# Kernel optimization log

Measured on AMD Instinct MI355X. Metric: run time of the kernel, lower is better.

Reference implementation:

```python
import jax, jax.numpy as jnp
import numpy as np

B_SZ, L, N, H = 8, 4096, 256, 256
R_MIN, R_MAX, MAX_PHASE = 0.0, 1.0, 0.314


def setup_inputs() -> dict:
    key = jax.random.key(0)
    ks = jax.random.split(key, 8)
    x = jax.random.normal(ks[0], (B_SZ, L, H), jnp.float32)
    def glorot(k, shape):
        return jax.random.normal(k, shape, jnp.float32) * jnp.sqrt(2.0 / (shape[0] + shape[1])).astype(jnp.float32)
    B_re = glorot(ks[1], (N, H))
    B_im = glorot(ks[2], (N, H))
    C_re = glorot(ks[3], (H, N))
    C_im = glorot(ks[4], (H, N))
    # DiskRingRadius / DiskRingPhase initializers
    u1 = jax.random.uniform(ks[5], (N,), jnp.float32, 1e-6, 1.0)
    u2 = jax.random.uniform(ks[6], (N,), jnp.float32, 1e-6, 1.0)
    nu_log = jnp.log(-0.5 * jnp.log(u1 * (R_MAX ** 2 - R_MIN ** 2) + R_MIN ** 2))
    theta_log = jnp.log(MAX_PHASE * u2)
    D = jax.random.normal(ks[7], (H,), jnp.float32) * 0.05  # RandomNormal(stddev=0.05)
    return dict(x=x, B_re=B_re, B_im=B_im, C_re=C_re, C_im=C_im,
                nu_log=nu_log, theta_log=theta_log, D=D)


def reference(x, B_re, B_im, C_re, C_im, nu_log, theta_log, D):
    # Diagonal complex recurrence parameters
    Lambda = jnp.exp(jax.lax.complex(-jnp.exp(nu_log), jnp.exp(theta_log)))  # [N]
    gamma = jnp.sqrt(1.0 - jnp.abs(Lambda) ** 2).astype(jnp.complex64)       # [N]
    B_norm = (B_re + 1j * B_im).astype(jnp.complex64) * gamma[:, None]       # [N,H]
    C = (C_re + 1j * C_im).astype(jnp.complex64)                             # [H,N]

    # Input projection: [B,L,N] complex
    Bu = jnp.einsum('blh,nh->bln', x.astype(jnp.complex64), B_norm)
    Lambda_el = jnp.broadcast_to(Lambda, Bu.shape)

    def combine(a, b):
        la, ba = a
        lb, bb = b
        return (la * lb, lb * ba + bb)

    _, states = jax.lax.associative_scan(combine, (Lambda_el, Bu), axis=1)  # [B,L,N]

    y = jnp.real(jnp.einsum('bln,hn->blh', states, C))
    y = y + x * D  # H_in == H -> elementwise skip
    return y
```

## Files before the change

### kernel.cpp

```cpp
#include <hip/hip_runtime.h>
#include <hip/hip_bf16.h>
#include <math.h>

#define B_SZ 8
#define LSEQ 4096
#define NDIM 256
#define HDIM 256
#define MROWS (B_SZ * LSEQ)
#define CH 64
#define NC (LSEQ / CH)

#define BM 64
#define BN 128
#define BK 32
#define PAD 40
#define SSTR 68

typedef _Float16 half8 __attribute__((ext_vector_type(8)));
typedef _Float16 half4 __attribute__((ext_vector_type(4)));
typedef float fx4 __attribute__((ext_vector_type(4)));

__global__ void k_prep(const float* __restrict__ Bre, const float* __restrict__ Bim,
                       const float* __restrict__ Cre, const float* __restrict__ Cim,
                       const float* __restrict__ nu_log, const float* __restrict__ th_log,
                       _Float16* __restrict__ BreH, _Float16* __restrict__ BimH,
                       _Float16* __restrict__ CreH, _Float16* __restrict__ CimNH,
                       float* __restrict__ lamRe, float* __restrict__ lamIm,
                       float* __restrict__ powRe, float* __restrict__ powIm) {
    int r = blockIdx.x;
    int t = threadIdx.x;
    float nu  = expf(nu_log[r]);
    float th  = expf(th_log[r]);
    float mod = expf(-nu);
    float g   = sqrtf(fmaxf(1.0f - mod * mod, 0.0f));
    if (t == 0) {
        lamRe[r] = mod * cosf(th);
        lamIm[r] = mod * sinf(th);
    }
    int i = r * 256 + t;
    BreH[i]  = (_Float16)(Bre[i] * g);
    BimH[i]  = (_Float16)(Bim[i] * g);
    CreH[i]  = (_Float16)Cre[i];
    CimNH[i] = (_Float16)(-Cim[i]);
    if (r < CH) {
        float nuN = expf(nu_log[t]);
        float thN = expf(th_log[t]);
        float k   = (float)(r + 1);
        float mo  = expf(-nuN * k);
        powRe[r * 256 + t] = mo * cosf(thN * k);
        powIm[r * 256 + t] = mo * sinf(thN * k);
    }
}

__launch_bounds__(256)
__global__ void k_buscan(const float* __restrict__ x,
                         const _Float16* __restrict__ BreH,
                         const _Float16* __restrict__ BimH,
                         const float* __restrict__ lamRe,
                         const float* __restrict__ lamIm,
                         _Float16* __restrict__ stReH,
                         _Float16* __restrict__ stImH,
                         float* __restrict__ finRe,
                         float* __restrict__ finIm) {
    __shared__ __align__(16) _Float16 smem[25600];

    const int tid  = threadIdx.x;
    const int lane = tid & 63;
    const int wave = tid >> 6;
    const int wr   = wave >> 1;
    const int wc   = wave & 1;
    const int m0   = blockIdx.x * BM;
    const int n0   = blockIdx.y * BN;

    const int ar = tid >> 2, ac = (tid & 3) * 8;
    const int br = tid >> 1, bc = (tid & 1) * 16;

    const int fRC = lane & 15;
    const int fKg = (lane >> 4) * 8;

    fx4 accR[8], accI[8];
#pragma unroll
    for (int i = 0; i < 8; ++i) { accR[i] = (fx4)0.0f; accI[i] = (fx4)0.0f; }

    float4 xf0, xf1;
    half8 w0, w1, w2, w3;

    {
        const float* xp = x + (size_t)(m0 + ar) * HDIM + ac;
        xf0 = *(const float4*)xp;
        xf1 = *(const float4*)(xp + 4);
        const _Float16* bp1 = BreH + (size_t)(n0 + br) * HDIM + bc;
        const _Float16* bp2 = BimH + (size_t)(n0 + br) * HDIM + bc;
        w0 = *(const half8*)bp1;  w1 = *(const half8*)(bp1 + 8);
        w2 = *(const half8*)bp2;  w3 = *(const half8*)(bp2 + 8);
        half8 hv;
        hv[0]=(_Float16)xf0.x; hv[1]=(_Float16)xf0.y; hv[2]=(_Float16)xf0.z; hv[3]=(_Float16)xf0.w;
        hv[4]=(_Float16)xf1.x; hv[5]=(_Float16)xf1.y; hv[6]=(_Float16)xf1.z; hv[7]=(_Float16)xf1.w;
        *(half8*)&smem[ar * PAD + ac] = hv;
        *(half8*)&smem[2560 + br * PAD + bc] = w0;  *(half8*)&smem[2560 + br * PAD + bc + 8] = w1;
        *(half8*)&smem[7680 + br * PAD + bc] = w2;  *(half8*)&smem[7680 + br * PAD + bc + 8] = w3;
    }
    __syncthreads();

    int p = 0;
    for (int k0 = 0; k0 < HDIM; k0 += BK) {
        const int po = p * 12800;
        const bool nx = (k0 + BK) < HDIM;
        if (nx) {
            const float* xp = x + (size_t)(m0 + ar) * HDIM + k0 + BK + ac;
            xf0 = *(const float4*)xp;
            xf1 = *(const float4*)(xp + 4);
            const _Float16* bp1 = BreH + (size_t)(n0 + br) * HDIM + k0 + BK + bc;
            const _Float16* bp2 = BimH + (size_t)(n0 + br) * HDIM + k0 + BK + bc;
            w0 = *(const half8*)bp1;  w1 = *(const half8*)(bp1 + 8);
            w2 = *(const half8*)bp2;  w3 = *(const half8*)(bp2 + 8);
        }
        half8 af[2], bRf[4], bIf[4];
#pragma unroll
        for (int sm = 0; sm < 2; ++sm)
            af[sm] = *(const half8*)&smem[po + (wr * 32 + sm * 16 + fRC) * PAD + fKg];
#pragma unroll
        for (int sn = 0; sn < 4; ++sn) {
            bRf[sn] = *(const half8*)&smem[po + 2560 + (wc * 64 + sn * 16 + fRC) * PAD + fKg];
            bIf[sn] = *(const half8*)&smem[po + 7680 + (wc * 64 + sn * 16 + fRC) * PAD + fKg];
        }
#pragma unroll
        for (int sm = 0; sm < 2; ++sm)
#pragma unroll
            for (int sn = 0; sn < 4; ++sn) {
                accR[sm * 4 + sn] = __builtin_amdgcn_mfma_f32_16x16x32_f16(af[sm], bRf[sn], accR[sm * 4 + sn], 0, 0, 0);
                accI[sm * 4 + sn] = __builtin_amdgcn_mfma_f32_16x16x32_f16(af[sm], bIf[sn], accI[sm * 4 + sn], 0, 0, 0);
            }
        if (nx) {
            const int qo = (p ^ 1) * 12800;
            half8 hv;
            hv[0]=(_Float16)xf0.x; hv[1]=(_Float16)xf0.y; hv[2]=(_Float16)xf0.z; hv[3]=(_Float16)xf0.w;
            hv[4]=(_Float16)xf1.x; hv[5]=(_Float16)xf1.y; hv[6]=(_Float16)xf1.z; hv[7]=(_Float16)xf1.w;
            *(half8*)&smem[qo + ar * PAD + ac] = hv;
            *(half8*)&smem[qo + 2560 + br * PAD + bc] = w0;  *(half8*)&smem[qo + 2560 + br * PAD + bc + 8] = w1;
            *(half8*)&smem[qo + 7680 + br * PAD + bc] = w2;  *(half8*)&smem[qo + 7680 + br * PAD + bc + 8] = w3;
        }
        __syncthreads();
        p ^= 1;
    }

    _Float16* SRe = smem;
    _Float16* SIm = smem + 8704;

    const int rBase = (lane >> 4) * 4;
#pragma unroll
    for (int sm = 0; sm < 2; ++sm)
#pragma unroll
        for (int sn = 0; sn < 4; ++sn) {
            int col = wc * 64 + sn * 16 + fRC;
            int row = wr * 32 + sm * 16 + rBase;
            half4 h1, h2;
#pragma unroll
            for (int reg = 0; reg < 4; ++reg) {
                h1[reg] = (_Float16)accR[sm * 4 + sn][reg];
                h2[reg] = (_Float16)accI[sm * 4 + sn][reg];
            }
            *(half4*)&SRe[col * SSTR + row] = h1;
            *(half4*)&SIm[col * SSTR + row] = h2;
        }
    __syncthreads();

    if (tid < BN) {
        int col = tid;
        int n = n0 + col;
        float lr = lamRe[n], li = lamIm[n];
        _Float16* cR = &SRe[col * SSTR];
        _Float16* cI = &SIm[col * SSTR];
        float sr = 0.0f, si = 0.0f;
#pragma unroll 8
        for (int r = 0; r < CH; ++r) {
            float ur = (float)cR[r];
            float ui = (float)cI[r];
            float nr = fmaf(lr, sr, fmaf(-li, si, ur));
            float ni = fmaf(lr, si, fmaf(li, sr, ui));
            sr = nr; si = ni;
            cR[r] = (_Float16)sr;
            cI[r] = (_Float16)si;
        }
        int bb = blockIdx.x >> 6, cc = blockIdx.x & 63;
        size_t f = ((size_t)(bb * NC + cc)) * NDIM + n;
        finRe[f] = sr;
        finIm[f] = si;
    }
    __syncthreads();

    {
        int row = tid >> 2;
        int cb  = (tid & 3) * 32;
        size_t gbase = (size_t)(m0 + row) * NDIM + n0 + cb;
#pragma unroll
        for (int g = 0; g < 4; ++g) {
            half8 h1, h2;
#pragma unroll
            for (int e = 0; e < 8; ++e) {
                int col = cb + g * 8 + e;
                h1[e] = SRe[col * SSTR + row];
                h2[e] = SIm[col * SSTR + row];
            }
            *(half8*)(stReH + gbase + g * 8) = h1;
            *(half8*)(stImH + gbase + g * 8) = h2;
        }
    }
}

__launch_bounds__(256)
__global__ void k_carry(const float* __restrict__ lamRe,
                        const float* __restrict__ lamIm,
                        const float* __restrict__ finRe,
                        const float* __restrict__ finIm,
                        float* __restrict__ carRe,
                        float* __restrict__ carIm) {
    const int b = blockIdx.x;
    const int n = threadIdx.x;
    const float lr = lamRe[n];
    const float li = lamIm[n];
    float kr = 1.0f, ki = 0.0f;
#pragma unroll
    for (int i = 0; i < CH; ++i) {
        float t = kr * lr - ki * li;
        ki = fmaf(kr, li, ki * lr);
        kr = t;
    }
    float cr = 0.0f, ci = 0.0f;
#pragma unroll 8
    for (int c = 0; c < NC; ++c) {
        size_t idx = ((size_t)b * NC + c) * NDIM + n;
        carRe[idx] = cr;
        carIm[idx] = ci;
        float fr = finRe[idx];
        float fi = finIm[idx];
        float t = fmaf(kr, cr, fmaf(-ki, ci, fr));
        ci = fmaf(kr, ci, fmaf(ki, cr, fi));
        cr = t;
    }
}

__launch_bounds__(256)
__global__ void k_out(const _Float16* __restrict__ sReH,
                      const _Float16* __restrict__ sImH,
                      const _Float16* __restrict__ CreH,
                      const _Float16* __restrict__ CimNH,
                      const float* __restrict__ powRe,
                      const float* __restrict__ powIm,
                      const float* __restrict__ carRe,
                      const float* __restrict__ carIm,
                      const float* __restrict__ x,
                      const float* __restrict__ Dv,
                      float* __restrict__ y) {
    __shared__ __align__(16) _Float16 A1[2][BM * PAD];
    __shared__ __align__(16) _Float16 A2[2][BM * PAD];
    __shared__ __align__(16) _Float16 Cr[2][BN * PAD];
    __shared__ __align__(16) _Float16 Ci[2][BN * PAD];

    const int tid  = threadIdx.x;
    const int lane = tid & 63;
    const int wave = tid >> 6;
    const int wr   = wave >> 1;
    const int wc   = wave & 1;
    const int m0   = blockIdx.x * BM;
    const int h0   = blockIdx.y * BN;
    const int chunk = m0 >> 6;

    const int ar = tid >> 2, ac = (tid & 3) * 8;
    const int br = tid >> 1, bc = (tid & 1) * 16;

    const int fRC = lane & 15;
    const int fKg = (lane >> 4) * 8;

    fx4 acc[8];
#pragma unroll
    for (int i = 0; i < 8; ++i) acc[i] = (fx4)0.0f;

    half8 s1, s2, c0a, c0b, c1a, c1b;
    float4 pr0, pr1, pi0, pi1, cr0, cr1, ci0, ci1;

#define LOAD_STAGE(K0)                                                          \
    {                                                                           \
        size_t aOff = (size_t)(m0 + ar) * NDIM + (K0) + ac;                     \
        s1 = *(const half8*)(sReH + aOff);                                      \
        s2 = *(const half8*)(sImH + aOff);                                      \
        size_t pOff = (size_t)ar * NDIM + (K0) + ac;                            \
        pr0 = *(const float4*)(powRe + pOff); pr1 = *(const float4*)(powRe + pOff + 4); \
        pi0 = *(const float4*)(powIm + pOff); pi1 = *(const float4*)(powIm + pOff + 4); \
        size_t cOff = (size_t)chunk * NDIM + (K0) + ac;                         \
        cr0 = *(const float4*)(carRe + cOff); cr1 = *(const float4*)(carRe + cOff + 4); \
        ci0 = *(const float4*)(carIm + cOff); ci1 = *(const float4*)(carIm + cOff + 4); \
        const _Float16* cp1 = CreH  + (size_t)(h0 + br) * NDIM + (K0) + bc;     \
        const _Float16* cp2 = CimNH + (size_t)(h0 + br) * NDIM + (K0) + bc;     \
        c0a = *(const half8*)cp1;  c0b = *(const half8*)(cp1 + 8);              \
        c1a = *(const half8*)cp2;  c1b = *(const half8*)(cp2 + 8);              \
    }

#define WRITE_STAGE(P)                                                          \
    {                                                                           \
        float prA[8] = {pr0.x,pr0.y,pr0.z,pr0.w,pr1.x,pr1.y,pr1.z,pr1.w};       \
        float piA[8] = {pi0.x,pi0.y,pi0.z,pi0.w,pi1.x,pi1.y,pi1.z,pi1.w};       \
        float crA[8] = {cr0.x,cr0.y,cr0.z,cr0.w,cr1.x,cr1.y,cr1.z,cr1.w};       \
        float ciA[8] = {ci0.x,ci0.y,ci0.z,ci0.w,ci1.x,ci1.y,ci1.z,ci1.w};       \
        half8 h1, h2;                                                           \
        _Pragma("unroll")                                                       \
        for (int e = 0; e < 8; ++e) {                                           \
            float ur = fmaf(prA[e], crA[e], fmaf(-piA[e], ciA[e], (float)s1[e])); \
            float ui = fmaf(prA[e], ciA[e], fmaf( piA[e], crA[e], (float)s2[e])); \
            h1[e] = (_Float16)ur; h2[e] = (_Float16)ui;                         \
        }                                                                       \
        *(half8*)&A1[P][ar * PAD + ac] = h1;                                    \
        *(half8*)&A2[P][ar * PAD + ac] = h2;                                    \
        *(half8*)&Cr[P][br * PAD + bc] = c0a;  *(half8*)&Cr[P][br * PAD + bc + 8] = c0b; \
        *(half8*)&Ci[P][br * PAD + bc] = c1a;  *(half8*)&Ci[P][br * PAD + bc + 8] = c1b; \
    }

    LOAD_STAGE(0);
    WRITE_STAGE(0);
    __syncthreads();

    int p = 0;
    for (int k0 = 0; k0 < NDIM; k0 += BK) {
        const bool nx = (k0 + BK) < NDIM;
        if (nx) LOAD_STAGE(k0 + BK);
        half8 a1[2], a2[2], bRf[4], bIf[4];
#pragma unroll
        for (int sm = 0; sm < 2; ++sm) {
            a1[sm] = *(const half8*)&A1[p][(wr * 32 + sm * 16 + fRC) * PAD + fKg];
            a2[sm] = *(const half8*)&A2[p][(wr * 32 + sm * 16 + fRC) * PAD + fKg];
        }
#pragma unroll
        for (int sn = 0; sn < 4; ++sn) {
            bRf[sn] = *(const half8*)&Cr[p][(wc * 64 + sn * 16 + fRC) * PAD + fKg];
            bIf[sn] = *(const half8*)&Ci[p][(wc * 64 + sn * 16 + fRC) * PAD + fKg];
        }
#pragma unroll
        for (int sm = 0; sm < 2; ++sm)
#pragma unroll
            for (int sn = 0; sn < 4; ++sn) {
                acc[sm * 4 + sn] = __builtin_amdgcn_mfma_f32_16x16x32_f16(a1[sm], bRf[sn], acc[sm * 4 + sn], 0, 0, 0);
                acc[sm * 4 + sn] = __builtin_amdgcn_mfma_f32_16x16x32_f16(a2[sm], bIf[sn], acc[sm * 4 + sn], 0, 0, 0);
            }
        if (nx) WRITE_STAGE(p ^ 1);
        __syncthreads();
        p ^= 1;
    }

    float d[4];
#pragma unroll
    for (int sn = 0; sn < 4; ++sn) d[sn] = Dv[h0 + wc * 64 + sn * 16 + fRC];

    const int rBase = (lane >> 4) * 4;
#pragma unroll
    for (int sm = 0; sm < 2; ++sm)
#pragma unroll
        for (int sn = 0; sn < 4; ++sn) {
            int h = h0 + wc * 64 + sn * 16 + fRC;
#pragma unroll
            for (int reg = 0; reg < 4; ++reg) {
                int m = m0 + wr * 32 + sm * 16 + rBase + reg;
                size_t idx = (size_t)m * HDIM + h;
                y[idx] = fmaf(x[idx], d[sn], acc[sm * 4 + sn][reg]);
            }
        }
#undef LOAD_STAGE
#undef WRITE_STAGE
}

extern "C" void kernel_launch(void* const* d_in, const int* in_sizes, int n_in,
                              void* d_out, int out_size, void* d_ws, size_t ws_size,
                              hipStream_t stream) {
    const float* x      = (const float*)d_in[0];
    const float* B_re   = (const float*)d_in[1];
    const float* B_im   = (const float*)d_in[2];
    const float* C_re   = (const float*)d_in[3];
    const float* C_im   = (const float*)d_in[4];
    const float* nu_log = (const float*)d_in[5];
    const float* th_log = (const float*)d_in[6];
    const float* D      = (const float*)d_in[7];
    float* y = (float*)d_out;

    char* p = (char*)d_ws;
    _Float16* stReH = (_Float16*)p;  p += (size_t)MROWS * NDIM * 2;
    _Float16* stImH = (_Float16*)p;  p += (size_t)MROWS * NDIM * 2;
    _Float16* BreH  = (_Float16*)p;  p += (size_t)NDIM * HDIM * 2;
    _Float16* BimH  = (_Float16*)p;  p += (size_t)NDIM * HDIM * 2;
    _Float16* CreH  = (_Float16*)p;  p += (size_t)HDIM * NDIM * 2;
    _Float16* CimNH = (_Float16*)p;  p += (size_t)HDIM * NDIM * 2;
    float* lamRe = (float*)p;  p += NDIM * 4;
    float* lamIm = (float*)p;  p += NDIM * 4;
    float* powRe = (float*)p;  p += (size_t)CH * NDIM * 4;
    float* powIm = (float*)p;  p += (size_t)CH * NDIM * 4;
    float* finRe = (float*)p;  p += (size_t)B_SZ * NC * NDIM * 4;
    float* finIm = (float*)p;  p += (size_t)B_SZ * NC * NDIM * 4;
    float* carRe = (float*)p;  p += (size_t)B_SZ * NC * NDIM * 4;
    float* carIm = (float*)p;  p += (size_t)B_SZ * NC * NDIM * 4;

    k_prep<<<NDIM, 256, 0, stream>>>(B_re, B_im, C_re, C_im, nu_log, th_log,
                                     BreH, BimH, CreH, CimNH, lamRe, lamIm,
                                     powRe, powIm);

    dim3 gGemm(MROWS / BM, NDIM / BN);
    k_buscan<<<gGemm, 256, 0, stream>>>(x, BreH, BimH, lamRe, lamIm,
                                        stReH, stImH, finRe, finIm);

    k_carry<<<B_SZ, 256, 0, stream>>>(lamRe, lamIm, finRe, finIm, carRe, carIm);

    dim3 gOut(MROWS / BM, HDIM / BN);
    k_out<<<gOut, 256, 0, stream>>>(stReH, stImH, CreH, CimNH,
                                    powRe, powIm, carRe, carIm, x, D, y);
}
```

Before: 161.8 us.

## Fold chunk carry computation into output GEMM via precomputed chunk powers

Removes the separate serial k_carry kernel, which ran only 8 blocks walking 64 chunks sequentially. Each output block now directly sums its incoming carry as a weighted reduction of earlier chunk finals times precomputed Lambda^(64k) powers, stores it in LDS and reads it from there. This saves a kernel launch and a low-parallelism serial stage. In exchange it adds redundant O(chunk index) work per block, repeated across both H tiles, and a different summation order that may affect numerics slightly.

```diff
diff --git a/kernel.cpp b/kernel.cpp
--- a/kernel.cpp
+++ b/kernel.cpp
@@ -26,7 +26,8 @@
                        _Float16* __restrict__ BreH, _Float16* __restrict__ BimH,
                        _Float16* __restrict__ CreH, _Float16* __restrict__ CimNH,
                        float* __restrict__ lamRe, float* __restrict__ lamIm,
-                       float* __restrict__ powRe, float* __restrict__ powIm) {
+                       float* __restrict__ powRe, float* __restrict__ powIm,
+                       float* __restrict__ powCRe, float* __restrict__ powCIm) {
     int r = blockIdx.x;
     int t = threadIdx.x;
     float nu  = expf(nu_log[r]);
@@ -42,13 +43,17 @@
     BimH[i]  = (_Float16)(Bim[i] * g);
     CreH[i]  = (_Float16)Cre[i];
     CimNH[i] = (_Float16)(-Cim[i]);
+    float nuN = expf(nu_log[t]);
+    float thN = expf(th_log[t]);
     if (r < CH) {
-        float nuN = expf(nu_log[t]);
-        float thN = expf(th_log[t]);
-        float k   = (float)(r + 1);
-        float mo  = expf(-nuN * k);
+        float k  = (float)(r + 1);
+        float mo = expf(-nuN * k);
         powRe[r * 256 + t] = mo * cosf(thN * k);
         powIm[r * 256 + t] = mo * sinf(thN * k);
+        float kc = (float)(CH * r);
+        float mc = expf(-nuN * kc);
+        powCRe[r * 256 + t] = mc * cosf(thN * kc);
+        powCIm[r * 256 + t] = mc * sinf(thN * kc);
     }
 }
 
@@ -209,46 +214,16 @@
 }
 
 __launch_bounds__(256)
-__global__ void k_carry(const float* __restrict__ lamRe,
-                        const float* __restrict__ lamIm,
-                        const float* __restrict__ finRe,
-                        const float* __restrict__ finIm,
-                        float* __restrict__ carRe,
-                        float* __restrict__ carIm) {
-    const int b = blockIdx.x;
-    const int n = threadIdx.x;
-    const float lr = lamRe[n];
-    const float li = lamIm[n];
-    float kr = 1.0f, ki = 0.0f;
-#pragma unroll
-    for (int i = 0; i < CH; ++i) {
-        float t = kr * lr - ki * li;
-        ki = fmaf(kr, li, ki * lr);
-        kr = t;
-    }
-    float cr = 0.0f, ci = 0.0f;
-#pragma unroll 8
-    for (int c = 0; c < NC; ++c) {
-        size_t idx = ((size_t)b * NC + c) * NDIM + n;
-        carRe[idx] = cr;
-        carIm[idx] = ci;
-        float fr = finRe[idx];
-        float fi = finIm[idx];
-        float t = fmaf(kr, cr, fmaf(-ki, ci, fr));
-        ci = fmaf(kr, ci, fmaf(ki, cr, fi));
-        cr = t;
-    }
-}
-
-__launch_bounds__(256)
 __global__ void k_out(const _Float16* __restrict__ sReH,
                       const _Float16* __restrict__ sImH,
                       const _Float16* __restrict__ CreH,
                       const _Float16* __restrict__ CimNH,
                       const float* __restrict__ powRe,
                       const float* __restrict__ powIm,
-                      const float* __restrict__ carRe,
-                      const float* __restrict__ carIm,
+                      const float* __restrict__ powCRe,
+                      const float* __restrict__ powCIm,
+                      const float* __restrict__ finRe,
+                      const float* __restrict__ finIm,
                       const float* __restrict__ x,
                       const float* __restrict__ Dv,
                       float* __restrict__ y) {
@@ -256,6 +231,7 @@
     __shared__ __align__(16) _Float16 A2[2][BM * PAD];
     __shared__ __align__(16) _Float16 Cr[2][BN * PAD];
     __shared__ __align__(16) _Float16 Ci[2][BN * PAD];
+    __shared__ __align__(16) float carL[2][NDIM];
 
     const int tid  = threadIdx.x;
     const int lane = tid & 63;
@@ -264,13 +240,33 @@
     const int wc   = wave & 1;
     const int m0   = blockIdx.x * BM;
     const int h0   = blockIdx.y * BN;
-    const int chunk = m0 >> 6;
+    const int bb   = blockIdx.x >> 6;
+    const int cc   = blockIdx.x & 63;
 
     const int ar = tid >> 2, ac = (tid & 3) * 8;
     const int br = tid >> 1, bc = (tid & 1) * 16;
 
     const int fRC = lane & 15;
     const int fKg = (lane >> 4) * 8;
+
+    {
+        const int n = tid;
+        float cr = 0.0f, ci = 0.0f;
+#pragma unroll 4
+        for (int j = 0; j < cc; ++j) {
+            int k = cc - 1 - j;
+            float pr = powCRe[k * NDIM + n];
+            float pi = powCIm[k * NDIM + n];
+            size_t f = ((size_t)(bb * NC + j)) * NDIM + n;
+            float fr = finRe[f];
+            float fi = finIm[f];
+            cr = fmaf(pr, fr, fmaf(-pi, fi, cr));
+            ci = fmaf(pr, fi, fmaf( pi, fr, ci));
+        }
+        carL[0][n] = cr;
+        carL[1][n] = ci;
+    }
+    __syncthreads();
 
     fx4 acc[8];
 #pragma unroll
@@ -287,9 +283,8 @@
         size_t pOff = (size_t)ar * NDIM + (K0) + ac;                            \
         pr0 = *(const float4*)(powRe + pOff); pr1 = *(const float4*)(powRe + pOff + 4); \
         pi0 = *(const float4*)(powIm + pOff); pi1 = *(const float4*)(powIm + pOff + 4); \
-        size_t cOff = (size_t)chunk * NDIM + (K0) + ac;                         \
-        cr0 = *(const float4*)(carRe + cOff); cr1 = *(const float4*)(carRe + cOff + 4); \
-        ci0 = *(const float4*)(carIm + cOff); ci1 = *(const float4*)(carIm + cOff + 4); \
+        cr0 = *(const float4*)&carL[0][(K0) + ac]; cr1 = *(const float4*)&carL[0][(K0) + ac + 4]; \
+        ci0 = *(const float4*)&carL[1][(K0) + ac]; ci1 = *(const float4*)&carL[1][(K0) + ac + 4]; \
         const _Float16* cp1 = CreH  + (size_t)(h0 + br) * NDIM + (K0) + bc;     \
         const _Float16* cp2 = CimNH + (size_t)(h0 + br) * NDIM + (K0) + bc;     \
         c0a = *(const half8*)cp1;  c0b = *(const half8*)(cp1 + 8);              \
@@ -387,26 +382,25 @@
     _Float16* BimH  = (_Float16*)p;  p += (size_t)NDIM * HDIM * 2;
     _Float16* CreH  = (_Float16*)p;  p += (size_t)HDIM * NDIM * 2;
     _Float16* CimNH = (_Float16*)p;  p += (size_t)HDIM * NDIM * 2;
-    float* lamRe = (float*)p;  p += NDIM * 4;
-    float* lamIm = (float*)p;  p += NDIM * 4;
-    float* powRe = (float*)p;  p += (size_t)CH * NDIM * 4;
-    float* powIm = (float*)p;  p += (size_t)CH * NDIM * 4;
-    float* finRe = (float*)p;  p += (size_t)B_SZ * NC * NDIM * 4;
-    float* finIm = (float*)p;  p += (size_t)B_SZ * NC * NDIM * 4;
-    float* carRe = (float*)p;  p += (size_t)B_SZ * NC * NDIM * 4;
-    float* carIm = (float*)p;  p += (size_t)B_SZ * NC * NDIM * 4;
+    float* lamRe  = (float*)p;  p += NDIM * 4;
+    float* lamIm  = (float*)p;  p += NDIM * 4;
+    float* powRe  = (float*)p;  p += (size_t)CH * NDIM * 4;
+    float* powIm  = (float*)p;  p += (size_t)CH * NDIM * 4;
+    float* powCRe = (float*)p;  p += (size_t)NC * NDIM * 4;
+    float* powCIm = (float*)p;  p += (size_t)NC * NDIM * 4;
+    float* finRe  = (float*)p;  p += (size_t)B_SZ * NC * NDIM * 4;
+    float* finIm  = (float*)p;  p += (size_t)B_SZ * NC * NDIM * 4;
 
     k_prep<<<NDIM, 256, 0, stream>>>(B_re, B_im, C_re, C_im, nu_log, th_log,
                                      BreH, BimH, CreH, CimNH, lamRe, lamIm,
-                                     powRe, powIm);
+                                     powRe, powIm, powCRe, powCIm);
 
     dim3 gGemm(MROWS / BM, NDIM / BN);
     k_buscan<<<gGemm, 256, 0, stream>>>(x, BreH, BimH, lamRe, lamIm,
                                         stReH, stImH, finRe, finIm);
 
-    k_carry<<<B_SZ, 256, 0, stream>>>(lamRe, lamIm, finRe, finIm, carRe, carIm);
-
     dim3 gOut(MROWS / BM, HDIM / BN);
     k_out<<<gOut, 256, 0, stream>>>(stReH, stImH, CreH, CimNH,
-                                    powRe, powIm, carRe, carIm, x, D, y);
+                                    powRe, powIm, powCRe, powCIm,
+                                    finRe, finIm, x, D, y);
 }
```

Result: no change. 164.0 us (+1.3%).
